# Performance work log

Hardware: AMD Instinct MI355X
Metric: run time of the kernel (lower is better)

Reference implementation:

```python
import jax, jax.numpy as jnp
import numpy as np

K = 51  # separable kernel taps
PAD = (K - 1) // 2  # 25


def _lerp_axis(a, n_in, n_out, axis):
    # 1D bilinear resample with align_corners=True semantics
    pos = jnp.arange(n_out, dtype=jnp.float32) * (float(n_in - 1) / float(n_out - 1))
    lo = jnp.floor(pos).astype(jnp.int32)
    hi = jnp.minimum(lo + 1, n_in - 1)
    w = (pos - lo.astype(jnp.float32)).astype(a.dtype)
    shp = [1] * a.ndim
    shp[axis] = n_out
    w = w.reshape(shp)
    return jnp.take(a, lo, axis=axis) * (1 - w) + jnp.take(a, hi, axis=axis) * w


def upsample2x_align_corners(x):
    B, C, H, W = x.shape
    x = _lerp_axis(x, H, 2 * H, 2)
    x = _lerp_axis(x, W, 2 * W, 3)
    return x


def conv3x3(x, w, b):
    y = jax.lax.conv_general_dilated(
        x, w, window_strides=(1, 1), padding=((1, 1), (1, 1)),
        dimension_numbers=('NCHW', 'OIHW', 'NCHW'))
    return y + b[None, :, None, None]


def kernel_block(x, w1, b1, w2, b2, w3, b3):
    h = upsample2x_align_corners(x)
    h = jax.nn.relu(conv3x3(h, w1, b1))
    h = jax.nn.relu(conv3x3(h, w2, b2))
    h = jax.nn.relu(conv3x3(h, w3, b3))
    return h  # [B, 51, H, W]


def sep_conv(img, kv, kh):
    # img: [B,C,H+K-1,W+K-1]; kv, kh: [B,K,H,W]
    # out[b,c,y,x] = sum_{i,j} img[b,c,y+i,x+j] * kv[b,i,y,x] * kh[b,j,y,x]
    B, C, Hp, Wp = img.shape
    H, W = kv.shape[2], kv.shape[3]
    # vertical sliding windows: [B,C,K,H,Wp]
    vwin = jnp.stack([img[:, :, i:i + H, :] for i in range(K)], axis=2)
    out = jnp.zeros((B, C, H, W), img.dtype)
    for j in range(K):  # static loop over K taps
        t = jnp.einsum('bciyx,biyx->bcyx', vwin[:, :, :, :, j:j + W], kv)
        out = out + t * kh[:, j][:, None]
    return out


def setup_inputs() -> dict:
    key = jax.random.key(0)
    ks = jax.random.split(key, 9)
    B, Cf, Hh, Wh = 4, 64, 128, 128  # feature map (half res)
    H, W = 2 * Hh, 2 * Wh
    x = jax.random.normal(ks[0], (B, Cf, Hh, Wh), jnp.float32)
    i1 = jax.random.normal(ks[1], (B, 3, H + 2 * PAD, W + 2 * PAD), jnp.float32)
    i2 = jax.random.normal(ks[2], (B, 3, H + 2 * PAD, W + 2 * PAD), jnp.float32)
    s = 0.05
    W1 = jax.random.normal(ks[3], (4, K, Cf, 3, 3), jnp.float32) * s
    B1 = jax.random.normal(ks[4], (4, K), jnp.float32) * s
    W2 = jax.random.normal(ks[5], (4, K, K, 3, 3), jnp.float32) * s
    B2 = jax.random.normal(ks[6], (4, K), jnp.float32) * s
    W3 = jax.random.normal(ks[7], (4, K, K, 3, 3), jnp.float32) * s
    B3 = jax.random.normal(ks[8], (4, K), jnp.float32) * s
    return {'x': x, 'i1': i1, 'i2': i2,
            'W1': W1, 'B1': B1, 'W2': W2, 'B2': B2, 'W3': W3, 'B3': B3}


def reference(x, i1, i2, W1, B1, W2, B2, W3, B3):
    kernels = [kernel_block(x, W1[k], B1[k], W2[k], B2[k], W3[k], B3[k])
               for k in range(4)]
    k1v, k1h, k2v, k2h = kernels
    y = sep_conv(i1, k1v, k1h) + sep_conv(i2, k2v, k2h)
    return y
```

## Files before the change

### kernel.cpp

```cpp
#include <hip/hip_runtime.h>
#include <stdint.h>

#define HH 128
#define H 256
#define W 256
#define KK 51
#define HIMG 306
#define WIMG 306
#define IMW 312
#define CF 64
#define BB 4
#define HWN (H * W)
#define CHAIN ((size_t)HWN * 64)

typedef short bhalf8 __attribute__((ext_vector_type(8)));
typedef float f32x4 __attribute__((ext_vector_type(4)));

__device__ inline uint16_t f2bf(float f) {
    uint32_t u = __builtin_bit_cast(uint32_t, f);
    u += 0x7FFF + ((u >> 16) & 1);
    return (uint16_t)(u >> 16);
}
__device__ inline float bf2f(uint16_t h) {
    uint32_t u = ((uint32_t)h) << 16;
    return __builtin_bit_cast(float, u);
}

__global__ __launch_bounds__(256) void upsample_cvt(const float* __restrict__ xin,
                                                    uint16_t* __restrict__ upT) {
    __shared__ float SU[2][64][19];
    const int y = blockIdx.x, x0 = blockIdx.y * 32;
    const float s = 127.f / 255.f;
    float py = y * s; int ly = (int)py; int hy = min(ly + 1, 127); float wy = py - (float)ly;
    int lx0 = (int)(x0 * s);
    for (int t = threadIdx.x; t < 2 * 64 * 18; t += 256) {
        int col = t % 18; int c = (t / 18) & 63; int row = t / (18 * 64);
        int sy = row ? hy : ly;
        int sx = min(lx0 + col, 127);
        SU[row][c][col] = xin[((size_t)c * 128 + sy) * 128 + sx];
    }
    __syncthreads();
    const int xl = threadIdx.x & 31, cg = threadIdx.x >> 5;
    const int x = x0 + xl;
    float px = x * s; int lx = (int)px; float wx = px - (float)lx;
    int lxl = lx - lx0;
    int hxl = min(lx + 1, 127) - lx0;
    uint32_t d[4];
#pragma unroll
    for (int q4 = 0; q4 < 4; ++q4) {
        uint32_t two[2];
#pragma unroll
        for (int e = 0; e < 2; ++e) {
            int c = cg * 8 + q4 * 2 + e;
            float v00 = SU[0][c][lxl], v01 = SU[0][c][hxl];
            float v10 = SU[1][c][lxl], v11 = SU[1][c][hxl];
            float a = v00 * (1.f - wy) + v10 * wy;
            float b = v01 * (1.f - wy) + v11 * wy;
            two[e] = f2bf(a * (1.f - wx) + b * wx);
        }
        d[q4] = two[0] | (two[1] << 16);
    }
    uint4 v = {d[0], d[1], d[2], d[3]};
    *(uint4*)(upT + ((size_t)y * W + x) * 64 + cg * 8) = v;
}

__global__ void img_cvt(const float* __restrict__ i1, const float* __restrict__ i2,
                        uint16_t* __restrict__ dst) {
    int task = blockIdx.x * 256 + threadIdx.x;
    if (task >= 7344 * 39) return;
    int ch8 = task % 39, row = task / 39;
    int u0 = ch8 * 8;
    int img = row / 3672;
    int r = row - img * 3672;
    const float* src = (img ? i2 : i1) + (size_t)r * WIMG;
    uint32_t d[4];
#pragma unroll
    for (int p = 0; p < 4; ++p) {
        int u = u0 + p * 2;
        uint32_t lo = (u < WIMG) ? f2bf(src[u]) : 0u;
        uint32_t hi = (u + 1 < WIMG) ? f2bf(src[u + 1]) : 0u;
        d[p] = lo | (hi << 16);
    }
    uint4 v = {d[0], d[1], d[2], d[3]};
    *(uint4*)(dst + (size_t)row * IMW + u0) = v;
}

__global__ void wprep(const float* __restrict__ wsrc, uint16_t* __restrict__ wdst, int cin_act) {
    int g = blockIdx.x * 256 + threadIdx.x;
    if (g >= 4 * 9 * 4 * 2 * 64) return;
    int lane = g & 63;
    int q = g >> 6;
    int ch = q & 1; q >>= 1;
    int m = q & 3; q >>= 2;
    int tap = q % 9;
    int k = q / 9;
    int co = m * 16 + (lane & 15);
    int ci0 = ch * 32 + (lane >> 4) * 8;
    uint32_t d[4];
#pragma unroll
    for (int p = 0; p < 4; ++p) {
        uint32_t w2[2];
#pragma unroll
        for (int e = 0; e < 2; ++e) {
            int ci = ci0 + p * 2 + e;
            float v = 0.f;
            if (co < KK && ci < cin_act)
                v = wsrc[((size_t)(k * KK + co) * cin_act + ci) * 9 + tap];
            w2[e] = f2bf(v);
        }
        d[p] = w2[0] | (w2[1] << 16);
    }
    uint4 v = {d[0], d[1], d[2], d[3]};
    *(uint4*)(wdst + (size_t)g * 8) = v;
}

__global__ __launch_bounds__(256, 2)
void conv_mfma(const uint16_t* __restrict__ in, const uint16_t* __restrict__ wp,
               const float* __restrict__ bias, uint16_t* __restrict__ out,
               size_t in_kstride, int kbase) {
    const int z = blockIdx.z;
    const int k = kbase + z;
    in  += (size_t)z * in_kstride;
    out += (size_t)z * CHAIN;
    const int y0 = blockIdx.x * 4;
    const int x0 = blockIdx.y * 128;
    const int tid = threadIdx.x;
    const int lane = tid & 63;
    const int wv = tid >> 6;
    const int y = y0 + wv;

    __shared__ uint4 lds[6 * 130 * 4];

    f32x4 acc[4][8];
#pragma unroll
    for (int m = 0; m < 4; ++m)
#pragma unroll
        for (int n = 0; n < 8; ++n)
            acc[m][n] = (f32x4){0.f, 0.f, 0.f, 0.f};

    for (int chf = 0; chf < 2; ++chf) {
        if (chf) __syncthreads();
        for (int task = tid; task < 6 * 130 * 4; task += 256) {
            int chunk = task & 3;
            int xl = (task >> 2) % 130;
            int r = (task >> 2) / 130;
            int yg = y0 - 1 + r;
            int xg = x0 + xl - 1;
            uint4 v = {0u, 0u, 0u, 0u};
            if ((unsigned)yg < H && (unsigned)xg < W)
                v = *(const uint4*)(in + (((size_t)yg * W + xg) * 64 + chf * 32 + chunk * 8));
            int slot = chunk ^ ((xl >> 1) & 3);
            lds[(r * 130 + xl) * 4 + slot] = v;
        }
        __syncthreads();

#pragma unroll
        for (int tap = 0; tap < 9; ++tap) {
            const int ky = tap / 3, kx = tap % 3;
            bhalf8 afr[4];
#pragma unroll
            for (int m = 0; m < 4; ++m)
                afr[m] = *(const bhalf8*)(wp + ((((size_t)(k * 9 + tap) * 4 + m) * 2 + chf) * 64 + lane) * 8);
            const int rrow = wv + ky;
            const int chunk = lane >> 4;
#pragma unroll
            for (int n = 0; n < 8; ++n) {
                int xl = n * 16 + (lane & 15) + kx;
                int slot = chunk ^ ((xl >> 1) & 3);
                bhalf8 bfr = *(const bhalf8*)&lds[(rrow * 130 + xl) * 4 + slot];
#pragma unroll
                for (int m = 0; m < 4; ++m)
                    acc[m][n] = __builtin_amdgcn_mfma_f32_16x16x32_bf16(afr[m], bfr, acc[m][n], 0, 0, 0);
            }
        }
    }

    __syncthreads();
    const int colx = lane & 15;
    const int r4 = lane >> 4;
    ushort* ST = (ushort*)lds + wv * 4096;
    float bv[4][4];
#pragma unroll
    for (int m = 0; m < 4; ++m)
#pragma unroll
        for (int r = 0; r < 4; ++r) {
            int co = m * 16 + r4 * 4 + r;
            bv[m][r] = (co < KK) ? bias[k * KK + co] : 0.f;
        }

#pragma unroll
    for (int ph = 0; ph < 2; ++ph) {
#pragma unroll
        for (int m = 0; m < 4; ++m) {
#pragma unroll
            for (int nn = 0; nn < 4; ++nn) {
                int n = ph * 4 + nn;
                int xl = nn * 16 + colx;
                uint32_t pk[2];
#pragma unroll
                for (int hh = 0; hh < 2; ++hh) {
                    uint32_t lo = f2bf(fmaxf(acc[m][n][hh * 2]     + bv[m][hh * 2],     0.f));
                    uint32_t hi = f2bf(fmaxf(acc[m][n][hh * 2 + 1] + bv[m][hh * 2 + 1], 0.f));
                    pk[hh] = lo | (hi << 16);
                }
                int co0 = m * 16 + r4 * 4;
                int idx = xl * 64 + (co0 ^ ((xl & 7) << 3));
                *(uint2*)(ST + idx) = (uint2){pk[0], pk[1]};
            }
        }
        const int p8 = lane >> 3;
        const int chunk = lane & 7;
#pragma unroll
        for (int it = 0; it < 8; ++it) {
            int px = it * 8 + p8;
            uint4 v = *(const uint4*)(ST + px * 64 + ((chunk ^ (px & 7)) << 3));
            int xg = x0 + ph * 64 + px;
            *(uint4*)(out + (((size_t)y * W + xg) * 64 + chunk * 8)) = v;
        }
    }
}

__global__ __launch_bounds__(256, 2)
void sepconv3(const uint16_t* __restrict__ imgb,
              const uint16_t* __restrict__ kvT, const uint16_t* __restrict__ khT,
              float* __restrict__ out, int accum) {
    __shared__ uint4 SB[320 * 8];
    __shared__ float SC[4][16 * 83];
    const int y = blockIdx.x, c = blockIdx.y;
    const int tid = threadIdx.x, lane = tid & 63, wv = tid >> 6;
    const uint16_t* img = imgb + (size_t)c * HIMG * IMW;

    for (int task = tid; task < 40 * 64; task += 256) {
        int i = task & 63;
        int u0 = (task >> 6) * 8;
        uint4 v = {0u, 0u, 0u, 0u};
        if (i <= 50 && u0 < IMW)
            v = *(const uint4*)(img + (size_t)(y + i) * IMW + u0);
        ushort* vs = (ushort*)&v;
#pragma unroll
        for (int e = 0; e < 8; ++e) {
            int u = u0 + e;
            *((ushort*)SB + u * 64 + (((i >> 3) ^ (u & 7)) << 3) + (i & 7)) = vs[e];
        }
    }
    __syncthreads();

    const int l4 = lane & 15, g = lane >> 4;
    for (int xt = 0; xt < 4; ++xt) {
        const int x0 = (wv * 4 + xt) * 16;
        const int xpix = x0 + l4;
        bhalf8 a0 = *(const bhalf8*)(kvT + ((size_t)y * W + xpix) * 64 + g * 8);
        bhalf8 a1 = *(const bhalf8*)(kvT + ((size_t)y * W + xpix) * 64 + 32 + g * 8);
        f32x4 acc[5];
#pragma unroll
        for (int nt = 0; nt < 5; ++nt) acc[nt] = (f32x4){0.f, 0.f, 0.f, 0.f};
#pragma unroll
        for (int nt = 0; nt < 5; ++nt) {
            int u = x0 + nt * 16 + l4;
            bhalf8 b0 = *(const bhalf8*)((ushort*)SB + u * 64 + ((g ^ (u & 7)) << 3));
            acc[nt] = __builtin_amdgcn_mfma_f32_16x16x32_bf16(a0, b0, acc[nt], 0, 0, 0);
            bhalf8 b1 = *(const bhalf8*)((ushort*)SB + u * 64 + (((4 + g) ^ (u & 7)) << 3));
            acc[nt] = __builtin_amdgcn_mfma_f32_16x16x32_bf16(a1, b1, acc[nt], 0, 0, 0);
        }
#pragma unroll
        for (int nt = 0; nt < 5; ++nt)
#pragma unroll
            for (int r = 0; r < 4; ++r)
                SC[wv][(g * 4 + r) * 83 + nt * 16 + l4] = acc[nt][r];

        const uint16_t* khp = khT + ((size_t)y * W + xpix) * 64;
        float partial = 0.f;
#pragma unroll
        for (int jj = 0; jj < 13; ++jj) {
            int j = g * 13 + jj;
            if (j < KK)
                partial = fmaf(SC[wv][l4 * 83 + l4 + j], bf2f(khp[j]), partial);
        }
        partial += __shfl_xor(partial, 16);
        partial += __shfl_xor(partial, 32);
        if (g == 0) {
            size_t oi = ((size_t)c * H + y) * W + xpix;
            if (accum) out[oi] += partial;
            else       out[oi] = partial;
        }
    }
}

extern "C" void kernel_launch(void* const* d_in, const int* in_sizes, int n_in,
                              void* d_out, int out_size, void* d_ws, size_t ws_size,
                              hipStream_t stream) {
    const float* x  = (const float*)d_in[0];
    const float* i1 = (const float*)d_in[1];
    const float* i2 = (const float*)d_in[2];
    const float* W1 = (const float*)d_in[3];
    const float* B1 = (const float*)d_in[4];
    const float* W2 = (const float*)d_in[5];
    const float* B2 = (const float*)d_in[6];
    const float* W3 = (const float*)d_in[7];
    const float* B3 = (const float*)d_in[8];
    float* out = (float*)d_out;

    char* wsb = (char*)d_ws;
    const size_t IMGB = CHAIN * 2;
    const size_t WPN  = 4 * 9 * 4 * 2 * 64 * 8;
    const size_t WPB  = WPN * 2;
    const size_t IMGBYTES = (size_t)2 * 4 * 3 * HIMG * IMW * 2;
    const size_t FULL_NEED = 13 * IMGB + 3 * WPB + IMGBYTES;
    const bool full = ws_size >= FULL_NEED;
    const int IMG_CVT_BLOCKS = (7344 * 39 + 255) / 256;

    if (full) {
        uint16_t* r1   = (uint16_t*)wsb;
        uint16_t* r2   = (uint16_t*)(wsb + 4 * IMGB);
        uint16_t* r3   = (uint16_t*)(wsb + 8 * IMGB);
        uint16_t* upT  = (uint16_t*)(wsb + 12 * IMGB);
        uint16_t* wp1  = (uint16_t*)(wsb + 13 * IMGB);
        uint16_t* wp2  = wp1 + WPN;
        uint16_t* wp3  = wp2 + WPN;
        uint16_t* imgb = wp3 + WPN;

        wprep<<<72, 256, 0, stream>>>(W1, wp1, CF);
        wprep<<<72, 256, 0, stream>>>(W2, wp2, KK);
        wprep<<<72, 256, 0, stream>>>(W3, wp3, KK);
        img_cvt<<<IMG_CVT_BLOCKS, 256, 0, stream>>>(i1, i2, imgb);

        for (int b = 0; b < BB; ++b) {
            upsample_cvt<<<dim3(H, 8), 256, 0, stream>>>(x + (size_t)b * CF * HH * HH, upT);
            conv_mfma<<<dim3(64, 2, 4), 256, 0, stream>>>(upT, wp1, B1, r1, 0, 0);
            conv_mfma<<<dim3(64, 2, 4), 256, 0, stream>>>(r1, wp2, B2, r2, CHAIN, 0);
            conv_mfma<<<dim3(64, 2, 4), 256, 0, stream>>>(r2, wp3, B3, r3, CHAIN, 0);
            for (int p = 0; p < 2; ++p) {
                const uint16_t* ib = imgb + ((size_t)(p * 12 + b * 3) * HIMG) * IMW;
                sepconv3<<<dim3(H, 3), 256, 0, stream>>>(ib,
                        r3 + (size_t)(2 * p) * CHAIN, r3 + (size_t)(2 * p + 1) * CHAIN,
                        out + (size_t)b * 3 * HWN, p);
            }
        }
    } else {
        uint16_t* upT  = (uint16_t*)wsb;
        uint16_t* t1   = (uint16_t*)(wsb + 1 * IMGB);
        uint16_t* t2   = (uint16_t*)(wsb + 3 * IMGB);
        uint16_t* t3   = (uint16_t*)(wsb + 5 * IMGB);
        uint16_t* wp1  = (uint16_t*)(wsb + 7 * IMGB);
        uint16_t* wp2  = wp1 + WPN;
        uint16_t* wp3  = wp2 + WPN;
        uint16_t* imgb = wp3 + WPN;

        wprep<<<72, 256, 0, stream>>>(W1, wp1, CF);
        wprep<<<72, 256, 0, stream>>>(W2, wp2, KK);
        wprep<<<72, 256, 0, stream>>>(W3, wp3, KK);
        img_cvt<<<IMG_CVT_BLOCKS, 256, 0, stream>>>(i1, i2, imgb);

        for (int b = 0; b < BB; ++b) {
            upsample_cvt<<<dim3(H, 8), 256, 0, stream>>>(x + (size_t)b * CF * HH * HH, upT);
            for (int p = 0; p < 2; ++p) {
                conv_mfma<<<dim3(64, 2, 2), 256, 0, stream>>>(upT, wp1, B1, t1, 0, 2 * p);
                conv_mfma<<<dim3(64, 2, 2), 256, 0, stream>>>(t1, wp2, B2, t2, CHAIN, 2 * p);
                conv_mfma<<<dim3(64, 2, 2), 256, 0, stream>>>(t2, wp3, B3, t3, CHAIN, 2 * p);
                const uint16_t* ib = imgb + ((size_t)(p * 12 + b * 3) * HIMG) * IMW;
                sepconv3<<<dim3(H, 3), 256, 0, stream>>>(ib, t3, t3 + CHAIN,
                        out + (size_t)b * 3 * HWN, p);
            }
        }
    }
}
```

Before: 590.7 us.

## Halve conv tile width, stage all 64 channels once via registers, raise MFMA priority

Each conv_mfma block now covers a 64-pixel-wide tile instead of 128. All 64 input channels are staged into LDS in one pass: global loads go into registers first and are then stored with a new XOR swizzle. This removes the second load phase and the barrier between the two channel halves. The accumulator array is halved, the MFMA loop runs under raised s_setprio, and the grid doubles in y. The aim is more blocks, lower register pressure and better overlap, at the cost of more halo reloading per output pixel.

```diff
diff --git a/kernel.cpp b/kernel.cpp
--- a/kernel.cpp
+++ b/kernel.cpp
@@ -123,37 +123,48 @@
     in  += (size_t)z * in_kstride;
     out += (size_t)z * CHAIN;
     const int y0 = blockIdx.x * 4;
-    const int x0 = blockIdx.y * 128;
+    const int x0 = blockIdx.y * 64;
     const int tid = threadIdx.x;
     const int lane = tid & 63;
     const int wv = tid >> 6;
     const int y = y0 + wv;
 
-    __shared__ uint4 lds[6 * 130 * 4];
-
-    f32x4 acc[4][8];
+    __shared__ uint4 lds[6 * 66 * 8];
+
+    uint4 stg[13];
+    int   dsti[13];
+#pragma unroll
+    for (int it = 0; it < 13; ++it) {
+        int t = tid + it * 256;
+        bool ok = t < 6 * 66 * 8;
+        int c = t & 7;
+        int q = t >> 3;
+        int xl = q % 66;
+        int r = q / 66;
+        int yg = y0 - 1 + r;
+        int xg = x0 + xl - 1;
+        uint4 v = {0u, 0u, 0u, 0u};
+        if (ok && (unsigned)yg < H && (unsigned)xg < W)
+            v = *(const uint4*)(in + (((size_t)yg * W + xg) * 64 + c * 8));
+        stg[it] = v;
+        dsti[it] = ok ? (q * 8 + (c ^ (xl & 7))) : -1;
+    }
+#pragma unroll
+    for (int it = 0; it < 13; ++it)
+        if (dsti[it] >= 0) lds[dsti[it]] = stg[it];
+    __syncthreads();
+
+    f32x4 acc[4][4];
 #pragma unroll
     for (int m = 0; m < 4; ++m)
 #pragma unroll
-        for (int n = 0; n < 8; ++n)
+        for (int n = 0; n < 4; ++n)
             acc[m][n] = (f32x4){0.f, 0.f, 0.f, 0.f};
 
+    const int l4 = lane & 15, g = lane >> 4;
+    __builtin_amdgcn_s_setprio(1);
+#pragma unroll
     for (int chf = 0; chf < 2; ++chf) {
-        if (chf) __syncthreads();
-        for (int task = tid; task < 6 * 130 * 4; task += 256) {
-            int chunk = task & 3;
-            int xl = (task >> 2) % 130;
-            int r = (task >> 2) / 130;
-            int yg = y0 - 1 + r;
-            int xg = x0 + xl - 1;
-            uint4 v = {0u, 0u, 0u, 0u};
-            if ((unsigned)yg < H && (unsigned)xg < W)
-                v = *(const uint4*)(in + (((size_t)yg * W + xg) * 64 + chf * 32 + chunk * 8));
-            int slot = chunk ^ ((xl >> 1) & 3);
-            lds[(r * 130 + xl) * 4 + slot] = v;
-        }
-        __syncthreads();
-
 #pragma unroll
         for (int tap = 0; tap < 9; ++tap) {
             const int ky = tap / 3, kx = tap % 3;
@@ -162,22 +173,22 @@
             for (int m = 0; m < 4; ++m)
                 afr[m] = *(const bhalf8*)(wp + ((((size_t)(k * 9 + tap) * 4 + m) * 2 + chf) * 64 + lane) * 8);
             const int rrow = wv + ky;
-            const int chunk = lane >> 4;
-#pragma unroll
-            for (int n = 0; n < 8; ++n) {
-                int xl = n * 16 + (lane & 15) + kx;
-                int slot = chunk ^ ((xl >> 1) & 3);
-                bhalf8 bfr = *(const bhalf8*)&lds[(rrow * 130 + xl) * 4 + slot];
+#pragma unroll
+            for (int n = 0; n < 4; ++n) {
+                int xl = n * 16 + l4 + kx;
+                int slot = (chf * 4 + g) ^ (xl & 7);
+                bhalf8 bfr = *(const bhalf8*)&lds[((size_t)rrow * 66 + xl) * 8 + slot];
 #pragma unroll
                 for (int m = 0; m < 4; ++m)
                     acc[m][n] = __builtin_amdgcn_mfma_f32_16x16x32_bf16(afr[m], bfr, acc[m][n], 0, 0, 0);
             }
         }
     }
+    __builtin_amdgcn_s_setprio(0);
 
     __syncthreads();
-    const int colx = lane & 15;
-    const int r4 = lane >> 4;
+    const int colx = l4;
+    const int r4 = g;
     ushort* ST = (ushort*)lds + wv * 4096;
     float bv[4][4];
 #pragma unroll
@@ -189,34 +200,28 @@
         }
 
 #pragma unroll
-    for (int ph = 0; ph < 2; ++ph) {
-#pragma unroll
-        for (int m = 0; m < 4; ++m) {
-#pragma unroll
-            for (int nn = 0; nn < 4; ++nn) {
-                int n = ph * 4 + nn;
-                int xl = nn * 16 + colx;
-                uint32_t pk[2];
-#pragma unroll
-                for (int hh = 0; hh < 2; ++hh) {
-                    uint32_t lo = f2bf(fmaxf(acc[m][n][hh * 2]     + bv[m][hh * 2],     0.f));
-                    uint32_t hi = f2bf(fmaxf(acc[m][n][hh * 2 + 1] + bv[m][hh * 2 + 1], 0.f));
-                    pk[hh] = lo | (hi << 16);
-                }
-                int co0 = m * 16 + r4 * 4;
-                int idx = xl * 64 + (co0 ^ ((xl & 7) << 3));
-                *(uint2*)(ST + idx) = (uint2){pk[0], pk[1]};
+    for (int m = 0; m < 4; ++m) {
+#pragma unroll
+        for (int nn = 0; nn < 4; ++nn) {
+            int xl = nn * 16 + colx;
+            uint32_t pk[2];
+#pragma unroll
+            for (int hh = 0; hh < 2; ++hh) {
+                uint32_t lo = f2bf(fmaxf(acc[m][nn][hh * 2]     + bv[m][hh * 2],     0.f));
+                uint32_t hi = f2bf(fmaxf(acc[m][nn][hh * 2 + 1] + bv[m][hh * 2 + 1], 0.f));
+                pk[hh] = lo | (hi << 16);
             }
-        }
-        const int p8 = lane >> 3;
-        const int chunk = lane & 7;
-#pragma unroll
-        for (int it = 0; it < 8; ++it) {
-            int px = it * 8 + p8;
-            uint4 v = *(const uint4*)(ST + px * 64 + ((chunk ^ (px & 7)) << 3));
-            int xg = x0 + ph * 64 + px;
-            *(uint4*)(out + (((size_t)y * W + xg) * 64 + chunk * 8)) = v;
-        }
+            int idx = xl * 64 + ((m * 16 + r4 * 4) ^ ((xl & 7) << 3));
+            *(uint2*)(ST + idx) = (uint2){pk[0], pk[1]};
+        }
+    }
+    const int p8 = lane >> 3;
+    const int ch = lane & 7;
+#pragma unroll
+    for (int it = 0; it < 8; ++it) {
+        int px = it * 8 + p8;
+        uint4 v = *(const uint4*)(ST + px * 64 + ((ch ^ (px & 7)) << 3));
+        *(uint4*)(out + (((size_t)y * W + x0 + px) * 64 + ch * 8)) = v;
     }
 }
 
@@ -326,9 +331,9 @@
 
         for (int b = 0; b < BB; ++b) {
             upsample_cvt<<<dim3(H, 8), 256, 0, stream>>>(x + (size_t)b * CF * HH * HH, upT);
-            conv_mfma<<<dim3(64, 2, 4), 256, 0, stream>>>(upT, wp1, B1, r1, 0, 0);
-            conv_mfma<<<dim3(64, 2, 4), 256, 0, stream>>>(r1, wp2, B2, r2, CHAIN, 0);
-            conv_mfma<<<dim3(64, 2, 4), 256, 0, stream>>>(r2, wp3, B3, r3, CHAIN, 0);
+            conv_mfma<<<dim3(64, 4, 4), 256, 0, stream>>>(upT, wp1, B1, r1, 0, 0);
+            conv_mfma<<<dim3(64, 4, 4), 256, 0, stream>>>(r1, wp2, B2, r2, CHAIN, 0);
+            conv_mfma<<<dim3(64, 4, 4), 256, 0, stream>>>(r2, wp3, B3, r3, CHAIN, 0);
             for (int p = 0; p < 2; ++p) {
                 const uint16_t* ib = imgb + ((size_t)(p * 12 + b * 3) * HIMG) * IMW;
                 sepconv3<<<dim3(H, 3), 256, 0, stream>>>(ib,
@@ -354,9 +359,9 @@
         for (int b = 0; b < BB; ++b) {
             upsample_cvt<<<dim3(H, 8), 256, 0, stream>>>(x + (size_t)b * CF * HH * HH, upT);
             for (int p = 0; p < 2; ++p) {
-                conv_mfma<<<dim3(64, 2, 2), 256, 0, stream>>>(upT, wp1, B1, t1, 0, 2 * p);
-                conv_mfma<<<dim3(64, 2, 2), 256, 0, stream>>>(t1, wp2, B2, t2, CHAIN, 2 * p);
-                conv_mfma<<<dim3(64, 2, 2), 256, 0, stream>>>(t2, wp3, B3, t3, CHAIN, 2 * p);
+                conv_mfma<<<dim3(64, 4, 2), 256, 0, stream>>>(upT, wp1, B1, t1, 0, 2 * p);
+                conv_mfma<<<dim3(64, 4, 2), 256, 0, stream>>>(t1, wp2, B2, t2, CHAIN, 2 * p);
+                conv_mfma<<<dim3(64, 4, 2), 256, 0, stream>>>(t2, wp3, B3, t3, CHAIN, 2 * p);
                 const uint16_t* ib = imgb + ((size_t)(p * 12 + b * 3) * HIMG) * IMW;
                 sepconv3<<<dim3(H, 3), 256, 0, stream>>>(ib, t3, t3 + CHAIN,
                         out + (size_t)b * 3 * HWN, p);
```

Result: no change. 595.2 us (+0.8%).
